# Kernel optimization log

Measured on AMD Instinct MI355X. Metric: run time of the kernel, lower is better.

The kernel has to match this reference:

```python
import jax, jax.numpy as jnp
import numpy as np

LN_EPS = 1e-5   # torch LayerNorm default
NRM_EPS = 1e-8  # normalizer-state epsilon in mLSTMCell


def setup_inputs() -> dict:
    key = jax.random.key(0)
    ks = jax.random.split(key, 3)
    B, T, H, L, O = 32, 256, 1024, 4, 256
    x = jax.random.normal(ks[0], (B, T, H), dtype=jnp.float32)
    # 6 projections per layer in order (q, k, v, i, f, o); Linear stored as [in, out]
    W = jax.random.normal(ks[1], (L, 6, H, H), dtype=jnp.float32) * 0.02
    b = jnp.zeros((L, 6, H), dtype=jnp.float32)
    ln_g = jnp.ones((L, 6, H), dtype=jnp.float32)
    ln_b = jnp.zeros((L, 6, H), dtype=jnp.float32)
    fc_w = jax.random.normal(ks[2], (H, O), dtype=jnp.float32) * 0.02
    fc_b = jnp.zeros((O,), dtype=jnp.float32)
    return {"x": x, "W": W, "b": b, "ln_g": ln_g, "ln_b": ln_b,
            "fc_w": fc_w, "fc_b": fc_b}


def _layer_norm(z, g, beta):
    # z: [6, B, H]; g, beta: [6, H]
    mu = z.mean(-1, keepdims=True)
    var = z.var(-1, keepdims=True)
    return (z - mu) * jax.lax.rsqrt(var + LN_EPS) * g[:, None, :] + beta[:, None, :]


def _cell(x_in, h_prev, c_prev, n_prev, Wl, bl, gl, betal):
    # x_in: [B, H]; states: [B, H]; Wl: [6, H, H]
    z = jnp.einsum('bh,jhd->jbd', x_in, Wl) + bl[:, None, :]
    z = _layer_norm(z, gl, betal)
    q, k, v, zi, zf, zo = z  # q is computed by the original cell but unused
    i = jnp.exp(zi)
    f = jax.nn.sigmoid(zf)
    o = jax.nn.sigmoid(zo)
    # kv_interaction = outer(k, v); sum over dim=1 == sum(k) * v (same math, no [B,H,H])
    kv_sum = k.sum(-1, keepdims=True) * v
    c = f * c_prev + i * kv_sum
    n = f * n_prev + i * k
    n_hat = n / (jnp.linalg.norm(n, axis=-1, keepdims=True) + NRM_EPS)
    h = o * jnp.tanh(c * n_hat)
    return h, c, n


def _mlstm_forward(x, W, b, ln_g, ln_b, fc_w, fc_b):
    B, T, H = x.shape
    L = W.shape[0]
    h0 = jnp.zeros((L, B, H), x.dtype)
    init = (h0, h0, h0)  # (h, c, n)

    def step(carry, x_t):
        h, c, n = carry
        layer_in = x_t
        hs, cs, ns = [], [], []
        for l in range(L):  # small fixed layer count
            h_l, c_l, n_l = _cell(layer_in, h[l], c[l], n[l],
                                  W[l], b[l], ln_g[l], ln_b[l])
            if l > 0:  # residual connection (use_residual=True)
                h_l = h_l + layer_in
            layer_in = h_l
            hs.append(h_l); cs.append(c_l); ns.append(n_l)
        return (jnp.stack(hs), jnp.stack(cs), jnp.stack(ns)), None

    (h, c, n), _ = jax.lax.scan(step, init, jnp.swapaxes(x, 0, 1))
    # output[-1] == top-layer hidden at the final timestep
    out = h[-1] @ fc_w + fc_b  # [B, O]
    return out, (h, c, n)


def reference(x, W, b, ln_g, ln_b, fc_w, fc_b):
    return _mlstm_forward(x, W, b, ln_g, ln_b, fc_w, fc_b)
```

## Files before the change

kernel.cpp:

```cpp
#include <hip/hip_runtime.h>
#include <hip/hip_bf16.h>
#include <math.h>

#define H 1024
#define B 32
#define T 256
#define L 4
#define O 256
#define SEGLEN 16
#define NSEG (T / SEGLEN)

typedef _Float16 half8 __attribute__((ext_vector_type(8)));
typedef _Float16 half4 __attribute__((ext_vector_type(4)));
typedef float f32x4 __attribute__((ext_vector_type(4)));

#define X_PK_OFF   0
#define HB0_OFF    8388608
#define HB1_OFF    16777216
#define WT2_OFF    25165824
#define Z16_OFF    46137344
#define SEGA_OFF   88080384
#define SEGBC_OFF  89128960
#define SEGBN_OFF  90177536
#define STATS_OFF  91226112
#define CARC_OFF   91422720
#define CARN_OFF   92471296
#define FCP_OFF    93519872

__device__ __forceinline__ void gll16(const _Float16* g, _Float16* l) {
  __builtin_amdgcn_global_load_lds(
      (const __attribute__((address_space(1))) void*)g,
      (__attribute__((address_space(3))) void*)l, 16, 0, 0);
}

__global__ __launch_bounds__(256) void pack_wx(
    const float* __restrict__ W, const float* __restrict__ x,
    _Float16* __restrict__ Wt2, _Float16* __restrict__ x_pk) {
  __shared__ float shmem[32 * 257];
  if (blockIdx.x < 5120) {
    int tile = blockIdx.x;
    int m_idx = tile >> 8;
    int kt = (tile >> 4) & 15, ntt = tile & 15;
    int l = m_idx / 5, jj = m_idx % 5;
    const float* Wf = W + ((size_t)(l * 6 + jj + 1) << 20);
    _Float16* out = Wt2 + ((size_t)m_idx << 20);
    float (*ts)[65] = (float(*)[65])shmem;
    int k0 = kt * 64, n0 = ntt * 64;
#pragma unroll
    for (int s = 0; s < 16; ++s) {
      int e = threadIdx.x + s * 256;
      int kk = e >> 6, col = e & 63;
      ts[kk][col] = Wf[(size_t)(k0 + kk) * H + n0 + col];
    }
    __syncthreads();
#pragma unroll
    for (int gi = 0; gi < 2; ++gi) {
      int g = threadIdx.x * 2 + gi;
      int l64 = g & 63, ksl = (g >> 6) & 1, ntl = g >> 7;
      int nn = l64 & 15, kh = l64 >> 4;
      half8 tmp;
#pragma unroll
      for (int e = 0; e < 8; ++e)
        tmp[e] = (_Float16)ts[ksl * 32 + kh * 8 + e][ntl * 16 + nn];
      *(half8*)&out[(size_t)((ntt * 4 + ntl) * 32 + kt * 2 + ksl) * 512 +
                    (size_t)l64 * 8] = tmp;
    }
  } else {
    int t = blockIdx.x - 5120;
    float (*ld)[257] = (float(*)[257])shmem;
    for (int c = 0; c < 4; ++c) {
      if (c) __syncthreads();
#pragma unroll
      for (int s = 0; s < 32; ++s) {
        int e2 = threadIdx.x + s * 256;
        int b = e2 >> 8, col = e2 & 255;
        ld[b][col] = x[((size_t)b * T + t) * H + c * 256 + col];
      }
      __syncthreads();
#pragma unroll
      for (int s3 = 0; s3 < 4; ++s3) {
        int gg = threadIdx.x * 4 + s3;
        int l64 = gg & 63, ksl = (gg >> 6) & 7, bt = gg >> 9;
        int nn = l64 & 15, kh = l64 >> 4;
        int b = bt * 16 + nn;
        half8 tmp;
#pragma unroll
        for (int e = 0; e < 8; ++e)
          tmp[e] = (_Float16)ld[b][ksl * 32 + kh * 8 + e];
        *(half8*)&x_pk[(size_t)t * 32768 + (size_t)bt * 16384 +
                       (size_t)(c * 8 + ksl) * 512 + (size_t)l64 * 8] = tmp;
      }
    }
  }
}

extern "C" __global__ __launch_bounds__(512, 1) void gemm_big(
    const _Float16* __restrict__ A_pk, const _Float16* __restrict__ Wl,
    _Float16* __restrict__ z16) {
  extern __shared__ _Float16 smem[];
  int raw = blockIdx.x;
  int xcd = raw & 7, c = raw >> 3;
  int bm = (xcd >> 1) * 8 + (c & 7);
  int bn = (xcd & 1) * 10 + (c >> 3);
  int w = threadIdx.x >> 6, lane = threadIdx.x & 63;
  int wm = w >> 2, wn = w & 3;
  int j = bn >> 2;

  const _Float16* gbase[8];
  int lbase[8];
#pragma unroll
  for (int q = 0; q < 8; ++q) {
    int f = w * 8 + q;
    if (f < 32) {
      int rm = f >> 1, ks2 = f & 1;
      gbase[q] = A_pk + (size_t)(bm * 16 + rm) * 16384 + (size_t)ks2 * 512 + lane * 8;
      lbase[q] = (rm * 2 + ks2) * 512;
    } else {
      int f2 = f - 32;
      int ntl = f2 >> 1, ks2 = f2 & 1;
      gbase[q] = Wl + ((size_t)j << 20) + (size_t)((bn & 3) * 16 + ntl) * 16384 +
                 (size_t)ks2 * 512 + lane * 8;
      lbase[q] = 16384 + (ntl * 2 + ks2) * 512;
    }
  }

#pragma unroll
  for (int q = 0; q < 8; ++q) gll16(gbase[q], &smem[lbase[q]]);
  asm volatile("s_waitcnt vmcnt(0)" ::: "memory");
  __builtin_amdgcn_s_barrier();
  __builtin_amdgcn_sched_barrier(0);

  f32x4 acc[8][4] = {};
  int abase = wm * 8 * 1024;
  int bbase = 16384 + wn * 4 * 1024;

  for (int kt = 0; kt < 16; ++kt) {
    int cur = (kt & 1) * 32768;
    int nxt = cur ^ 32768;
    half8 b[4][2];
#pragma unroll
    for (int jf = 0; jf < 4; ++jf)
#pragma unroll
      for (int k2 = 0; k2 < 2; ++k2)
        b[jf][k2] = *(const half8*)&smem[cur + bbase + (jf * 2 + k2) * 512 + lane * 8];
#pragma unroll
    for (int p = 0; p < 4; ++p) {
      if (p < 2 && kt + 1 < 16) {
#pragma unroll
        for (int q = 0; q < 4; ++q)
          gll16(gbase[p * 4 + q] + (size_t)(kt + 1) * 1024,
                &smem[nxt + lbase[p * 4 + q]]);
      }
      half8 a[2][2];
#pragma unroll
      for (int i2 = 0; i2 < 2; ++i2)
#pragma unroll
        for (int k2 = 0; k2 < 2; ++k2)
          a[i2][k2] = *(const half8*)&smem[cur + abase + ((p * 2 + i2) * 2 + k2) * 512 + lane * 8];
#pragma unroll
      for (int i2 = 0; i2 < 2; ++i2)
#pragma unroll
        for (int jf = 0; jf < 4; ++jf)
#pragma unroll
          for (int k2 = 0; k2 < 2; ++k2)
            acc[p * 2 + i2][jf] = __builtin_amdgcn_mfma_f32_16x16x32_f16(
                a[i2][k2], b[jf][k2], acc[p * 2 + i2][jf], 0, 0, 0);
    }
    asm volatile("s_waitcnt vmcnt(0) lgkmcnt(0)" ::: "memory");
    __builtin_amdgcn_s_barrier();
    __builtin_amdgcn_sched_barrier(0);
  }
  __syncthreads();

  _Float16 (*cz)[264] = (_Float16(*)[264])smem;
  int hb0 = (bn & 3) * 256;
  for (int g = 0; g < 4; ++g) {
    if (g) __syncthreads();
    if (wm == (g >> 1)) {
#pragma unroll
      for (int r4 = 0; r4 < 4; ++r4) {
        int fi = (g & 1) * 4 + r4;
#pragma unroll
        for (int jf = 0; jf < 4; ++jf)
#pragma unroll
          for (int r = 0; r < 4; ++r)
            cz[r4 * 16 + (lane >> 4) * 4 + r][wn * 64 + jf * 16 + (lane & 15)] =
                (_Float16)acc[fi][jf][r];
      }
    }
    __syncthreads();
#pragma unroll
    for (int s = 0; s < 4; ++s) {
      int e = threadIdx.x + s * 512;
      int r = e >> 5, h8 = e & 31;
      int m_local = bm * 256 + g * 64 + r;
      half8 vv = *(const half8*)&cz[r][h8 * 8];
      *(half8*)&z16[((size_t)m_local * 5 + j) * 1024 + hb0 + h8 * 8] = vv;
    }
  }
}

__global__ __launch_bounds__(256) void stats_kernel(
    const _Float16* __restrict__ z16, const float* __restrict__ bias,
    const float* __restrict__ ln_g, const float* __restrict__ ln_b,
    float* __restrict__ stats, int l) {
  int row = blockIdx.x, tid = threadIdx.x;
  int h0 = tid * 4;
  float red[13];
#pragma unroll
  for (int jj = 0; jj < 5; ++jj) {
    half4 z4 = *(const half4*)&z16[((size_t)row * 5 + jj) * 1024 + h0];
    float4 bb = *(const float4*)&bias[(size_t)(l * 6 + 1 + jj) * H + h0];
    float vx = (float)z4[0] + bb.x, vy = (float)z4[1] + bb.y,
          vz = (float)z4[2] + bb.z, vw = (float)z4[3] + bb.w;
    red[jj * 2] = vx + vy + vz + vw;
    red[jj * 2 + 1] = vx * vx + vy * vy + vz * vz + vw * vw;
    if (jj == 0) {
      float4 g = *(const float4*)&ln_g[(size_t)(l * 6 + 1) * H + h0];
      float4 be = *(const float4*)&ln_b[(size_t)(l * 6 + 1) * H + h0];
      red[10] = vx * g.x + vy * g.y + vz * g.z + vw * g.w;
      red[11] = g.x + g.y + g.z + g.w;
      red[12] = be.x + be.y + be.z + be.w;
    }
  }
#pragma unroll
  for (int off = 32; off; off >>= 1)
#pragma unroll
    for (int q = 0; q < 13; ++q) red[q] += __shfl_down(red[q], off);
  __shared__ float sb[4][13];
  if ((tid & 63) == 0) {
#pragma unroll
    for (int q = 0; q < 13; ++q) sb[tid >> 6][q] = red[q];
  }
  __syncthreads();
  if (tid == 0) {
    float st[13];
#pragma unroll
    for (int q = 0; q < 13; ++q) st[q] = sb[0][q] + sb[1][q] + sb[2][q] + sb[3][q];
    float* so = stats + (size_t)row * 12;
#pragma unroll
    for (int jj = 0; jj < 5; ++jj) {
      float mu = st[jj * 2] * (1.0f / H);
      float var = st[jj * 2 + 1] * (1.0f / H) - mu * mu;
      so[jj * 2] = mu;
      so[jj * 2 + 1] = rsqrtf(var + 1e-5f);
    }
    float mu0 = st[0] * (1.0f / H);
    float rs0 = rsqrtf(st[1] * (1.0f / H) - mu0 * mu0 + 1e-5f);
    so[10] = rs0 * (st[10] - mu0 * st[11]) + st[12];
    so[11] = 0.f;
  }
}

__global__ __launch_bounds__(256) void scan_p1agg(
    const _Float16* __restrict__ z16, const float* __restrict__ stats,
    const float* __restrict__ bias, const float* __restrict__ ln_g,
    const float* __restrict__ ln_b, float* __restrict__ segA,
    float* __restrict__ segBc, float* __restrict__ segBn, int l) {
  int idx = blockIdx.x * 256 + threadIdx.x;
  int h = idx & 1023;
  int bs = idx >> 10;
  int b = bs & 31, seg = bs >> 5;

  float bz[4], gg[4], bb[4];
#pragma unroll
  for (int jj = 0; jj < 4; ++jj) {
    bz[jj] = bias[(size_t)(l * 6 + 1 + jj) * H + h];
    gg[jj] = ln_g[(size_t)(l * 6 + 1 + jj) * H + h];
    bb[jj] = ln_b[(size_t)(l * 6 + 1 + jj) * H + h];
  }
  float A = 1.f, bc = 0.f, bn = 0.f;
#pragma unroll 2
  for (int u = 0; u < SEGLEN; ++u) {
    int row = (seg * SEGLEN + u) * 32 + b;
    size_t zb = ((size_t)row * 5) * 1024 + h;
    float zk = (float)z16[zb];
    float zv = (float)z16[zb + 1024];
    float zi = (float)z16[zb + 2048];
    float zf = (float)z16[zb + 3072];
    const float* st = stats + (size_t)row * 12;
    float k   = (zk + bz[0] - st[0]) * st[1] * gg[0] + bb[0];
    float v   = (zv + bz[1] - st[2]) * st[3] * gg[1] + bb[1];
    float zi_ = (zi + bz[2] - st[4]) * st[5] * gg[2] + bb[2];
    float zf_ = (zf + bz[3] - st[6]) * st[7] * gg[3] + bb[3];
    float iv = __expf(zi_);
    float fv = 1.f / (1.f + __expf(-zf_));
    A *= fv;
    bn = fv * bn + iv * k;
    bc = fv * bc + iv * (st[10] * v);
  }
  size_t so = ((size_t)seg * 32 + b) * 1024 + h;
  segA[so] = A;
  segBn[so] = bn;
  segBc[so] = bc;
}

__global__ __launch_bounds__(256) void scan_p2(
    const float* __restrict__ segA, const float* __restrict__ segBc,
    const float* __restrict__ segBn, float* __restrict__ carC,
    float* __restrict__ carN) {
  int idx = blockIdx.x * 256 + threadIdx.x;
  int h = idx & 1023, b = idx >> 10;
  float cc = 0.f, nn = 0.f;
#pragma unroll
  for (int seg = 0; seg < NSEG; ++seg) {
    size_t coff = (size_t)seg * 32768 + (size_t)b * 1024 + h;
    carC[coff] = cc;
    carN[coff] = nn;
    size_t so = ((size_t)seg * 32 + b) * 1024 + h;
    float a = segA[so];
    cc = segBc[so] + a * cc;
    nn = segBn[so] + a * nn;
  }
}

__global__ __launch_bounds__(256) void final_scan(
    const _Float16* __restrict__ z16, const float* __restrict__ stats,
    const float* __restrict__ bias, const float* __restrict__ ln_g,
    const float* __restrict__ ln_b, const float* __restrict__ carC,
    const float* __restrict__ carN, const _Float16* __restrict__ hin,
    _Float16* __restrict__ hout, float* __restrict__ out, int l) {
  int seg = blockIdx.x >> 5, b = blockIdx.x & 31;
  int tid = threadIdx.x, h0 = tid * 4;

  float bz[5][4], gg[5][4], bb[5][4];
#pragma unroll
  for (int jj = 0; jj < 5; ++jj) {
    float4 t1 = *(const float4*)&bias[(size_t)(l * 6 + 1 + jj) * H + h0];
    float4 t2 = *(const float4*)&ln_g[(size_t)(l * 6 + 1 + jj) * H + h0];
    float4 t3 = *(const float4*)&ln_b[(size_t)(l * 6 + 1 + jj) * H + h0];
    bz[jj][0] = t1.x; bz[jj][1] = t1.y; bz[jj][2] = t1.z; bz[jj][3] = t1.w;
    gg[jj][0] = t2.x; gg[jj][1] = t2.y; gg[jj][2] = t2.z; gg[jj][3] = t2.w;
    bb[jj][0] = t3.x; bb[jj][1] = t3.y; bb[jj][2] = t3.z; bb[jj][3] = t3.w;
  }

  size_t coff = (size_t)seg * 32768 + (size_t)b * 1024 + h0;
  float4 cC4 = *(const float4*)&carC[coff];
  float4 cN4 = *(const float4*)&carN[coff];
  float c_[4] = {cC4.x, cC4.y, cC4.z, cC4.w};
  float n_[4] = {cN4.x, cN4.y, cN4.z, cN4.w};

  size_t hfoff = (size_t)(b >> 4) * 16384 + (size_t)(h0 >> 5) * 512 +
                 (size_t)((((h0 & 31) >> 3) * 16) + (b & 15)) * 8 + (h0 & 7);
  __shared__ float sbuf[2][4];

  half4 zr[5];
  {
    int row0 = (seg * SEGLEN) * 32 + b;
#pragma unroll
    for (int jj = 0; jj < 5; ++jj)
      zr[jj] = *(const half4*)&z16[((size_t)row0 * 5 + jj) * 1024 + h0];
  }

  for (int u = 0; u < SEGLEN; ++u) {
    int t = seg * SEGLEN + u;
    int row = t * 32 + b;
    half4 zc[5];
#pragma unroll
    for (int jj = 0; jj < 5; ++jj) zc[jj] = zr[jj];
    if (u + 1 < SEGLEN) {
      int rown = (t + 1) * 32 + b;
#pragma unroll
      for (int jj = 0; jj < 5; ++jj)
        zr[jj] = *(const half4*)&z16[((size_t)rown * 5 + jj) * 1024 + h0];
    }
    half4 rin;
    if (l > 0) rin = *(const half4*)&hin[(size_t)t * 32768 + hfoff];

    const float* st = stats + (size_t)row * 12;
    float mu0 = st[0], rs0 = st[1], mu1 = st[2], rs1 = st[3];
    float mu2 = st[4], rs2 = st[5], mu3 = st[6], rs3 = st[7];
    float mu4 = st[8], rs4 = st[9], ksum = st[10];

    float ss = 0.f;
#pragma unroll
    for (int e = 0; e < 4; ++e) {
      float k   = ((float)zc[0][e] + bz[0][e] - mu0) * rs0 * gg[0][e] + bb[0][e];
      float v   = ((float)zc[1][e] + bz[1][e] - mu1) * rs1 * gg[1][e] + bb[1][e];
      float zi_ = ((float)zc[2][e] + bz[2][e] - mu2) * rs2 * gg[2][e] + bb[2][e];
      float zf_ = ((float)zc[3][e] + bz[3][e] - mu3) * rs3 * gg[3][e] + bb[3][e];
      float iv = __expf(zi_);
      float fv = 1.f / (1.f + __expf(-zf_));
      n_[e] = fv * n_[e] + iv * k;
      c_[e] = fv * c_[e] + iv * (ksum * v);
      ss += n_[e] * n_[e];
    }
#pragma unroll
    for (int off = 32; off; off >>= 1) ss += __shfl_down(ss, off);
    if ((tid & 63) == 0) sbuf[u & 1][tid >> 6] = ss;
    __syncthreads();
    float nrm = sbuf[u & 1][0] + sbuf[u & 1][1] + sbuf[u & 1][2] + sbuf[u & 1][3];
    float rn = 1.f / (sqrtf(nrm) + 1e-8f);

    float hh[4];
#pragma unroll
    for (int e = 0; e < 4; ++e) {
      float zo_ = ((float)zc[4][e] + bz[4][e] - mu4) * rs4 * gg[4][e] + bb[4][e];
      float ov = 1.f / (1.f + __expf(-zo_));
      float targ = c_[e] * (n_[e] * rn);
      float e2 = __expf(-2.f * fabsf(targ));
      float th = copysignf((1.f - e2) / (1.f + e2), targ);
      hh[e] = ov * th + ((l > 0) ? (float)rin[e] : 0.f);
    }
    half4 hx;
    hx[0] = (_Float16)hh[0]; hx[1] = (_Float16)hh[1];
    hx[2] = (_Float16)hh[2]; hx[3] = (_Float16)hh[3];
    *(half4*)&hout[(size_t)t * 32768 + hfoff] = hx;

    if (t == T - 1) {
      *(float4*)&out[8192 + (size_t)l * 32768 + (size_t)b * 1024 + h0] =
          make_float4(hh[0], hh[1], hh[2], hh[3]);
      *(float4*)&out[8192 + 131072 + ((size_t)(l * B) + b) * 1024 + h0] =
          make_float4(c_[0], c_[1], c_[2], c_[3]);
      *(float4*)&out[8192 + 262144 + ((size_t)(l * B) + b) * 1024 + h0] =
          make_float4(n_[0], n_[1], n_[2], n_[3]);
    }
  }
}

__global__ __launch_bounds__(256) void fc_part(
    const float* __restrict__ out_h, const float* __restrict__ fc_w,
    float* __restrict__ partial) {
  int b = blockIdx.x >> 3, kh = blockIdx.x & 7;
  int o = threadIdx.x;
  const float* hr = out_h + (size_t)b * 1024 + kh * 128;
  const float* wp = fc_w + (size_t)kh * 128 * O + o;
  float acc = 0.f;
#pragma unroll 8
  for (int h = 0; h < 128; ++h)
    acc = fmaf(hr[h], wp[(size_t)h * O], acc);
  partial[((size_t)kh * 32 + b) * O + o] = acc;
}

__global__ __launch_bounds__(256) void fc_reduce(
    const float* __restrict__ partial, const float* __restrict__ fc_b,
    float* __restrict__ out) {
  int b = blockIdx.x, o = threadIdx.x;
  float acc = fc_b[o];
#pragma unroll
  for (int kh = 0; kh < 8; ++kh)
    acc += partial[((size_t)kh * 32 + b) * O + o];
  out[(size_t)b * O + o] = acc;
}

extern "C" void kernel_launch(void* const* d_in, const int* in_sizes, int n_in,
                              void* d_out, int out_size, void* d_ws, size_t ws_size,
                              hipStream_t stream) {
  const float* x    = (const float*)d_in[0];
  const float* W    = (const float*)d_in[1];
  const float* bias = (const float*)d_in[2];
  const float* ln_g = (const float*)d_in[3];
  const float* ln_b = (const float*)d_in[4];
  const float* fc_w = (const float*)d_in[5];
  const float* fc_b = (const float*)d_in[6];
  float* out = (float*)d_out;
  _Float16* wsh = (_Float16*)d_ws;

  _Float16* x_pk = wsh + X_PK_OFF;
  _Float16* hb[2] = {wsh + HB0_OFF, wsh + HB1_OFF};
  _Float16* Wt2  = wsh + WT2_OFF;
  _Float16* z16  = wsh + Z16_OFF;
  float* segA  = (float*)(wsh + SEGA_OFF);
  float* segBc = (float*)(wsh + SEGBC_OFF);
  float* segBn = (float*)(wsh + SEGBN_OFF);
  float* stats = (float*)(wsh + STATS_OFF);
  float* carC  = (float*)(wsh + CARC_OFF);
  float* carN  = (float*)(wsh + CARN_OFF);
  float* fcp   = (float*)(wsh + FCP_OFF);

  static bool attr_set = false;
  if (!attr_set) {
    (void)hipFuncSetAttribute((const void*)gemm_big,
                              hipFuncAttributeMaxDynamicSharedMemorySize, 131072);
    attr_set = true;
  }

  pack_wx<<<5376, 256, 0, stream>>>(W, x, Wt2, x_pk);

  for (int l = 0; l < L; ++l) {
    const _Float16* A_in = (l == 0) ? x_pk : hb[(l - 1) & 1];
    _Float16* h_out = hb[l & 1];
    const _Float16* Wl = Wt2 + ((size_t)(l * 5) << 20);
    gemm_big<<<640, 512, 131072, stream>>>(A_in, Wl, z16);
    stats_kernel<<<8192, 256, 0, stream>>>(z16, bias, ln_g, ln_b, stats, l);
    scan_p1agg<<<2048, 256, 0, stream>>>(z16, stats, bias, ln_g, ln_b,
                                         segA, segBc, segBn, l);
    scan_p2<<<128, 256, 0, stream>>>(segA, segBc, segBn, carC, carN);
    final_scan<<<512, 256, 0, stream>>>(z16, stats, bias, ln_g, ln_b,
                                        carC, carN, A_in, h_out, out, l);
  }
  fc_part<<<256, 256, 0, stream>>>(out + 8192 + 3 * 32768, fc_w, fcp);
  fc_reduce<<<B, 256, 0, stream>>>(fcp, fc_b, out);
}
```

Baseline: 795.8 us.

## Restructure GEMM main loop into 4-slot, 3-deep software pipeline with half-K steps

The gemm_big main loop now advances in 32 half-width K steps over a 4-slot ring of shared-memory buffers instead of 16 full steps with double buffering. Each step issues async global-to-LDS loads two steps ahead and uses vmcnt partial waits, so loads stay in flight across compute. The aim is to hide global memory latency better than the old scheme, which drained all loads with vmcnt(0) every iteration. The trade-off is more barriers per K and fewer MFMAs between them. The host also now calls the shared-memory attribute setter unconditionally, adding a small per-call host API cost.

```diff
diff --git a/kernel.cpp b/kernel.cpp
--- a/kernel.cpp
+++ b/kernel.cpp
@@ -106,69 +106,69 @@
   int wm = w >> 2, wn = w & 3;
   int j = bn >> 2;
 
-  const _Float16* gbase[8];
-  int lbase[8];
-#pragma unroll
-  for (int q = 0; q < 8; ++q) {
-    int f = w * 8 + q;
-    if (f < 32) {
-      int rm = f >> 1, ks2 = f & 1;
-      gbase[q] = A_pk + (size_t)(bm * 16 + rm) * 16384 + (size_t)ks2 * 512 + lane * 8;
-      lbase[q] = (rm * 2 + ks2) * 512;
+  const _Float16* gbase[4];
+  int lbase[4];
+#pragma unroll
+  for (int q = 0; q < 4; ++q) {
+    int f = w * 4 + q;
+    if (f < 16) {
+      gbase[q] = A_pk + (size_t)(bm * 16 + f) * 16384 + lane * 8;
+      lbase[q] = f * 512 + lane * 8;
     } else {
-      int f2 = f - 32;
-      int ntl = f2 >> 1, ks2 = f2 & 1;
-      gbase[q] = Wl + ((size_t)j << 20) + (size_t)((bn & 3) * 16 + ntl) * 16384 +
-                 (size_t)ks2 * 512 + lane * 8;
-      lbase[q] = 16384 + (ntl * 2 + ks2) * 512;
-    }
-  }
-
-#pragma unroll
-  for (int q = 0; q < 8; ++q) gll16(gbase[q], &smem[lbase[q]]);
-  asm volatile("s_waitcnt vmcnt(0)" ::: "memory");
-  __builtin_amdgcn_s_barrier();
-  __builtin_amdgcn_sched_barrier(0);
+      int nf = f - 16;
+      gbase[q] = Wl + ((size_t)j << 20) + (size_t)((bn & 3) * 16 + nf) * 16384 + lane * 8;
+      lbase[q] = 8192 + nf * 512 + lane * 8;
+    }
+  }
+
+#pragma unroll
+  for (int h = 0; h < 2; ++h)
+#pragma unroll
+    for (int q = 0; q < 4; ++q)
+      gll16(gbase[q] + (size_t)h * 512, &smem[h * 16384 + lbase[q]]);
 
   f32x4 acc[8][4] = {};
-  int abase = wm * 8 * 1024;
-  int bbase = 16384 + wn * 4 * 1024;
-
-  for (int kt = 0; kt < 16; ++kt) {
-    int cur = (kt & 1) * 32768;
-    int nxt = cur ^ 32768;
-    half8 b[4][2];
+  int ard = wm * 4096 + lane * 8;
+  int brd = 8192 + wn * 2048 + lane * 8;
+
+  auto compute = [&](int h) {
+    int slot = (h & 3) * 16384;
+    half8 bfr[4], afr[8];
 #pragma unroll
     for (int jf = 0; jf < 4; ++jf)
-#pragma unroll
-      for (int k2 = 0; k2 < 2; ++k2)
-        b[jf][k2] = *(const half8*)&smem[cur + bbase + (jf * 2 + k2) * 512 + lane * 8];
-#pragma unroll
-    for (int p = 0; p < 4; ++p) {
-      if (p < 2 && kt + 1 < 16) {
-#pragma unroll
-        for (int q = 0; q < 4; ++q)
-          gll16(gbase[p * 4 + q] + (size_t)(kt + 1) * 1024,
-                &smem[nxt + lbase[p * 4 + q]]);
-      }
-      half8 a[2][2];
-#pragma unroll
-      for (int i2 = 0; i2 < 2; ++i2)
-#pragma unroll
-        for (int k2 = 0; k2 < 2; ++k2)
-          a[i2][k2] = *(const half8*)&smem[cur + abase + ((p * 2 + i2) * 2 + k2) * 512 + lane * 8];
-#pragma unroll
-      for (int i2 = 0; i2 < 2; ++i2)
-#pragma unroll
-        for (int jf = 0; jf < 4; ++jf)
-#pragma unroll
-          for (int k2 = 0; k2 < 2; ++k2)
-            acc[p * 2 + i2][jf] = __builtin_amdgcn_mfma_f32_16x16x32_f16(
-                a[i2][k2], b[jf][k2], acc[p * 2 + i2][jf], 0, 0, 0);
-    }
-    asm volatile("s_waitcnt vmcnt(0) lgkmcnt(0)" ::: "memory");
+      bfr[jf] = *(const half8*)&smem[slot + brd + jf * 512];
+#pragma unroll
+    for (int ri = 0; ri < 8; ++ri)
+      afr[ri] = *(const half8*)&smem[slot + ard + ri * 512];
+#pragma unroll
+    for (int ri = 0; ri < 8; ++ri)
+#pragma unroll
+      for (int jf = 0; jf < 4; ++jf)
+        acc[ri][jf] = __builtin_amdgcn_mfma_f32_16x16x32_f16(
+            afr[ri], bfr[jf], acc[ri][jf], 0, 0, 0);
+  };
+
+  for (int h = 0; h < 30; ++h) {
+#pragma unroll
+    for (int q = 0; q < 4; ++q)
+      gll16(gbase[q] + (size_t)(h + 2) * 512,
+            &smem[((h + 2) & 3) * 16384 + lbase[q]]);
+    asm volatile("s_waitcnt vmcnt(8)" ::: "memory");
     __builtin_amdgcn_s_barrier();
     __builtin_amdgcn_sched_barrier(0);
+    compute(h);
+  }
+  {
+    asm volatile("s_waitcnt vmcnt(4)" ::: "memory");
+    __builtin_amdgcn_s_barrier();
+    __builtin_amdgcn_sched_barrier(0);
+    compute(30);
+  }
+  {
+    asm volatile("s_waitcnt vmcnt(0)" ::: "memory");
+    __builtin_amdgcn_s_barrier();
+    __builtin_amdgcn_sched_barrier(0);
+    compute(31);
   }
   __syncthreads();
 
@@ -468,12 +468,8 @@
   float* carN  = (float*)(wsh + CARN_OFF);
   float* fcp   = (float*)(wsh + FCP_OFF);
 
-  static bool attr_set = false;
-  if (!attr_set) {
-    (void)hipFuncSetAttribute((const void*)gemm_big,
-                              hipFuncAttributeMaxDynamicSharedMemorySize, 131072);
-    attr_set = true;
-  }
+  (void)hipFuncSetAttribute((const void*)gemm_big,
+                            hipFuncAttributeMaxDynamicSharedMemorySize, 131072);
 
   pack_wx<<<5376, 256, 0, stream>>>(W, x, Wt2, x_pk);
 
```

New measurement: 784.1 us. Within noise of the previous version (-1.5%).
